# Kernel tuning notes

Hardware: AMD Instinct MI355X
Metric: run time of the kernel (lower is better)

Reference implementation:

```python
import jax, jax.numpy as jnp
import numpy as np

N_NODES = 50000
N_EDGES = 1600000
X_DIM = 128
HID = 128
HEADS = 8
C1 = HID // HEADS  # 16 per-head channels in gnn1
N_GRAPHS = 500
SLOPE = 0.3       # negative_slope (alpha in source)
BN_EPS = 1e-5


def segment_softmax(e, idx, n):
    # numerically stable softmax over segments defined by idx
    m = jax.ops.segment_max(e, idx, num_segments=n)
    ex = jnp.exp(e - m[idx])
    s = jax.ops.segment_sum(ex, idx, num_segments=n)
    return ex / (s[idx] + 1e-16)


def gatv2(x, src, dst, Wl, Wr, att, bias, heads, ch, concat):
    # PyG GATv2Conv (share_weights=False, edge_dim=None), eval mode (no dropout)
    n = x.shape[0]
    xl = (x @ Wl).reshape(n, heads, ch)  # messages (source side)
    xr = (x @ Wr).reshape(n, heads, ch)  # target side
    h = jax.nn.leaky_relu(xl[src] + xr[dst], SLOPE)      # [E,H,C]
    score = jnp.einsum('ehc,hc->eh', h, att)             # [E,H]
    alpha = segment_softmax(score, dst, n)               # softmax over in-edges of each target
    out = jax.ops.segment_sum(xl[src] * alpha[:, :, None], dst, num_segments=n)  # [N,H,C]
    out = out.reshape(n, heads * ch) if concat else out.mean(axis=1)
    return out + bias


def batchnorm_eval(x, g, b, rm, rv):
    return (x - rm) * (g / jnp.sqrt(rv + BN_EPS)) + b


def setup_inputs() -> dict:
    key = jax.random.key(0)
    ks = jax.random.split(key, 16)
    s = 0.05
    return {
        'x': jax.random.normal(ks[0], (N_NODES, X_DIM), jnp.float32),
        'edge_index': jax.random.randint(ks[1], (2, N_EDGES), 0, N_NODES, jnp.int32),
        'batch': jnp.sort(jax.random.randint(ks[2], (N_NODES,), 0, N_GRAPHS, jnp.int32)),
        # gnn1: GATv2Conv(x_dim -> hid//8, heads=8, concat)
        'Wl1': jax.random.normal(ks[3], (X_DIM, HID), jnp.float32) * s,
        'Wr1': jax.random.normal(ks[4], (X_DIM, HID), jnp.float32) * s,
        'att1': jax.random.normal(ks[5], (HEADS, C1), jnp.float32) * s,
        'b1': jnp.zeros((HID,), jnp.float32),
        # gnn2: GATv2Conv(hid -> hid, heads=1, concat=False)
        'Wl2': jax.random.normal(ks[6], (HID, HID), jnp.float32) * s,
        'Wr2': jax.random.normal(ks[7], (HID, HID), jnp.float32) * s,
        'att2': jax.random.normal(ks[8], (1, HID), jnp.float32) * s,
        'b2': jnp.zeros((HID,), jnp.float32),
        # shared BatchNorm1d(hid), eval mode buffers + affine
        'bn_g': jnp.ones((HID,), jnp.float32),
        'bn_b': jnp.zeros((HID,), jnp.float32),
        'bn_rm': jnp.zeros((HID,), jnp.float32),
        'bn_rv': jnp.ones((HID,), jnp.float32),
        # attentional aggregation gate_nn: Linear->Tanh->Linear(no bias)
        'Wg1': jax.random.normal(ks[9], (HID, HID), jnp.float32) * s,
        'bg1': jnp.zeros((HID,), jnp.float32),
        'Wg2': jax.random.normal(ks[10], (HID, 1), jnp.float32) * s,
        # fc_out: Linear(hid,100)->ReLU->Linear(100,1)
        'Wf1': jax.random.normal(ks[11], (HID, 100), jnp.float32) * s,
        'bf1': jnp.zeros((100,), jnp.float32),
        'Wf2': jax.random.normal(ks[12], (100, 1), jnp.float32) * s,
        'bf2': jnp.zeros((1,), jnp.float32),
    }


def reference(x, edge_index, batch, Wl1, Wr1, att1, b1, Wl2, Wr2, att2, b2,
              bn_g, bn_b, bn_rm, bn_rv, Wg1, bg1, Wg2, Wf1, bf1, Wf2, bf2):
    src, dst = edge_index[0], edge_index[1]
    # GAT layer 1 (8 heads, concat) -> dropout(eval no-op) -> BN -> ReLU
    h1 = gatv2(x, src, dst, Wl1, Wr1, att1, b1, HEADS, C1, True)
    h1 = jax.nn.relu(batchnorm_eval(h1, bn_g, bn_b, bn_rm, bn_rv))
    # GAT layer 2 (1 head, mean/no-concat) -> BN -> ReLU
    h2 = gatv2(h1, src, dst, Wl2, Wr2, att2, b2, 1, HID, False)
    h2 = jax.nn.relu(batchnorm_eval(h2, bn_g, bn_b, bn_rm, bn_rv))
    # AttentionalAggregation: softmax(gate_nn(x), batch) weighted sum
    gate = jnp.tanh(h2 @ Wg1 + bg1) @ Wg2                 # [N,1]
    gate = segment_softmax(gate, batch, N_GRAPHS)
    pooled = jax.ops.segment_sum(gate * h2, batch, num_segments=N_GRAPHS)  # [B,HID]
    # fc_out head
    return jax.nn.relu(pooled @ Wf1 + bf1) @ Wf2 + bf2    # [B,1]
```

## Files before the change

kernel.cpp:

```cpp
#include <hip/hip_runtime.h>
#include <math.h>

#define NEG_SLOPE 0.3f
#define BN_EPS 1e-5f
#define DEG_CAP 96

static __device__ __forceinline__ int lower_bound_i(const int* __restrict__ a, int n, int v) {
  int lo = 0, hi = n;
  while (lo < hi) {
    int mid = (lo + hi) >> 1;
    if (a[mid] < v) lo = mid + 1; else hi = mid;
  }
  return lo;
}

__global__ __launch_bounds__(256) void gemm2_kernel(const float* __restrict__ A,
    const float* __restrict__ W1, const float* __restrict__ W2,
    float* __restrict__ C1, float* __restrict__ C2, int n,
    const int* __restrict__ src, const int* __restrict__ dst, int ne,
    int* __restrict__ cursor, int* __restrict__ csr_src,
    const float* __restrict__ b1, const float* __restrict__ b2,
    const float* __restrict__ g, const float* __restrict__ bb,
    const float* __restrict__ rm, const float* __restrict__ rv,
    float* __restrict__ s1, float* __restrict__ h1s,
    float* __restrict__ s2, float* __restrict__ h2s,
    int gemm_blocks, int total_gs) {
  __shared__ float As[64 * 128];
  if (blockIdx.x >= total_gs) {
    int t = threadIdx.x;
    int c = t & 127;
    float s = g[c] / sqrtf(rv[c] + BN_EPS);
    const float* bias = (t < 128) ? b1 : b2;
    float* so = (t < 128) ? s1 : s2;
    float* ho = (t < 128) ? h1s : h2s;
    so[c] = s;
    ho[c] = (bias[c] - rm[c]) * s + bb[c];
    return;
  }
  if (blockIdx.x >= gemm_blocks) {
    int tid = (blockIdx.x - gemm_blocks) * 256 + threadIdx.x;
    int stride = (total_gs - gemm_blocks) * 256;
    int nb4 = ne >> 2;
    const int4* s4p = (const int4*)src;
    const int4* d4p = (const int4*)dst;
    for (int i = tid; i < nb4; i += stride) {
      int4 s4 = s4p[i];
      int4 d4 = d4p[i];
      csr_src[d4.x * DEG_CAP + atomicAdd(&cursor[d4.x], 1)] = s4.x;
      csr_src[d4.y * DEG_CAP + atomicAdd(&cursor[d4.y], 1)] = s4.y;
      csr_src[d4.z * DEG_CAP + atomicAdd(&cursor[d4.z], 1)] = s4.z;
      csr_src[d4.w * DEG_CAP + atomicAdd(&cursor[d4.w], 1)] = s4.w;
    }
    for (int i = (nb4 << 2) + tid; i < ne; i += stride) {
      int d = dst[i];
      csr_src[d * DEG_CAP + atomicAdd(&cursor[d], 1)] = src[i];
    }
    return;
  }
  int t = threadIdx.x;
  int r0 = blockIdx.x << 6;
  {
    float4* Asv = (float4*)As;
    if (r0 + 64 <= n) {
      const float4* Av = (const float4*)(A + (size_t)r0 * 128);
#pragma unroll
      for (int i = 0; i < 8; ++i) Asv[t + 256 * i] = Av[t + 256 * i];
    } else {
#pragma unroll
      for (int i = 0; i < 8; ++i) {
        int idx = t + 256 * i;
        int rr = idx >> 5;
        int cc = idx & 31;
        int gr = min(r0 + rr, n - 1);
        Asv[idx] = ((const float4*)(A + (size_t)gr * 128))[cc];
      }
    }
  }
  __syncthreads();
  int cg = t & 31;
  int rg = t >> 5;
  const float4* W1v = (const float4*)W1;
  const float4* W2v = (const float4*)W2;
  float4 a1[8], a2[8];
#pragma unroll
  for (int r = 0; r < 8; ++r) {
    a1[r] = make_float4(0.f, 0.f, 0.f, 0.f);
    a2[r] = make_float4(0.f, 0.f, 0.f, 0.f);
  }
  float4 u0 = W1v[0 * 32 + cg], u1 = W1v[1 * 32 + cg];
  float4 u2 = W1v[2 * 32 + cg], u3 = W1v[3 * 32 + cg];
  float4 v0 = W2v[0 * 32 + cg], v1 = W2v[1 * 32 + cg];
  float4 v2 = W2v[2 * 32 + cg], v3 = W2v[3 * 32 + cg];
#pragma unroll 2
  for (int kg = 0; kg < 32; ++kg) {
    int k = kg << 2;
    int kn = (kg < 31) ? (k + 4) : 0;
    float4 nu0 = W1v[(kn + 0) * 32 + cg];
    float4 nu1 = W1v[(kn + 1) * 32 + cg];
    float4 nu2 = W1v[(kn + 2) * 32 + cg];
    float4 nu3 = W1v[(kn + 3) * 32 + cg];
    float4 nv0 = W2v[(kn + 0) * 32 + cg];
    float4 nv1 = W2v[(kn + 1) * 32 + cg];
    float4 nv2 = W2v[(kn + 2) * 32 + cg];
    float4 nv3 = W2v[(kn + 3) * 32 + cg];
#pragma unroll
    for (int r = 0; r < 8; ++r) {
      float4 av = *(const float4*)&As[(rg * 8 + r) * 128 + k];
      a1[r].x += av.x * u0.x + av.y * u1.x + av.z * u2.x + av.w * u3.x;
      a1[r].y += av.x * u0.y + av.y * u1.y + av.z * u2.y + av.w * u3.y;
      a1[r].z += av.x * u0.z + av.y * u1.z + av.z * u2.z + av.w * u3.z;
      a1[r].w += av.x * u0.w + av.y * u1.w + av.z * u2.w + av.w * u3.w;
      a2[r].x += av.x * v0.x + av.y * v1.x + av.z * v2.x + av.w * v3.x;
      a2[r].y += av.x * v0.y + av.y * v1.y + av.z * v2.y + av.w * v3.y;
      a2[r].z += av.x * v0.z + av.y * v1.z + av.z * v2.z + av.w * v3.z;
      a2[r].w += av.x * v0.w + av.y * v1.w + av.z * v2.w + av.w * v3.w;
    }
    u0 = nu0; u1 = nu1; u2 = nu2; u3 = nu3;
    v0 = nv0; v1 = nv1; v2 = nv2; v3 = nv3;
  }
#pragma unroll
  for (int r = 0; r < 8; ++r) {
    int gr = r0 + rg * 8 + r;
    if (gr < n) {
      *(float4*)&C1[(size_t)gr * 128 + cg * 4] = a1[r];
      *(float4*)&C2[(size_t)gr * 128 + cg * 4] = a2[r];
    }
  }
}

__global__ __launch_bounds__(256) void gate_kernel(const float* __restrict__ A,
    const float* __restrict__ Wg1, const float* __restrict__ bg1,
    const float* __restrict__ Wg2, float* __restrict__ gate, int n) {
  __shared__ float As[64 * 128];
  int t = threadIdx.x;
  int r0 = blockIdx.x << 6;
  {
    float4* Asv = (float4*)As;
    if (r0 + 64 <= n) {
      const float4* Av = (const float4*)(A + (size_t)r0 * 128);
#pragma unroll
      for (int i = 0; i < 8; ++i) Asv[t + 256 * i] = Av[t + 256 * i];
    } else {
#pragma unroll
      for (int i = 0; i < 8; ++i) {
        int idx = t + 256 * i;
        int rr = idx >> 5;
        int cc = idx & 31;
        int gr = min(r0 + rr, n - 1);
        Asv[idx] = ((const float4*)(A + (size_t)gr * 128))[cc];
      }
    }
  }
  __syncthreads();
  int cg = t & 31;
  int rg = t >> 5;
  const float4* Wv = (const float4*)Wg1;
  float4 bg4 = *(const float4*)&bg1[cg * 4];
  float4 wg4 = *(const float4*)&Wg2[cg * 4];
  float4 acc[8];
#pragma unroll
  for (int r = 0; r < 8; ++r) acc[r] = make_float4(0.f, 0.f, 0.f, 0.f);
  float4 w0 = Wv[0 * 32 + cg];
  float4 w1 = Wv[1 * 32 + cg];
  float4 w2 = Wv[2 * 32 + cg];
  float4 w3 = Wv[3 * 32 + cg];
#pragma unroll 4
  for (int kg = 0; kg < 32; ++kg) {
    int k = kg << 2;
    int kn = (kg < 31) ? (k + 4) : 0;
    float4 nw0 = Wv[(kn + 0) * 32 + cg];
    float4 nw1 = Wv[(kn + 1) * 32 + cg];
    float4 nw2 = Wv[(kn + 2) * 32 + cg];
    float4 nw3 = Wv[(kn + 3) * 32 + cg];
#pragma unroll
    for (int r = 0; r < 8; ++r) {
      float4 av = *(const float4*)&As[(rg * 8 + r) * 128 + k];
      acc[r].x += av.x * w0.x + av.y * w1.x + av.z * w2.x + av.w * w3.x;
      acc[r].y += av.x * w0.y + av.y * w1.y + av.z * w2.y + av.w * w3.y;
      acc[r].z += av.x * w0.z + av.y * w1.z + av.z * w2.z + av.w * w3.z;
      acc[r].w += av.x * w0.w + av.y * w1.w + av.z * w2.w + av.w * w3.w;
    }
    w0 = nw0; w1 = nw1; w2 = nw2; w3 = nw3;
  }
#pragma unroll
  for (int r = 0; r < 8; ++r) {
    float v = tanhf(acc[r].x + bg4.x) * wg4.x
            + tanhf(acc[r].y + bg4.y) * wg4.y
            + tanhf(acc[r].z + bg4.z) * wg4.z
            + tanhf(acc[r].w + bg4.w) * wg4.w;
    v += __shfl_xor(v, 1);
    v += __shfl_xor(v, 2);
    v += __shfl_xor(v, 4);
    v += __shfl_xor(v, 8);
    v += __shfl_xor(v, 16);
    int gr = r0 + rg * 8 + r;
    if (cg == 0 && gr < n) gate[gr] = v;
  }
}

template<bool REDUCE>
__global__ __launch_bounds__(64) void gat_fused(
    const float* __restrict__ xl, const float* __restrict__ xr,
    const int* __restrict__ csr_src, const int* __restrict__ deg,
    const float* __restrict__ att,
    const float* __restrict__ bnscale, const float* __restrict__ bnshift,
    float* __restrict__ out, int n_nodes) {
  int n = blockIdx.x;
  if (n >= n_nodes) return;
  int l = threadIdx.x;
  int c = l & 7;
  int es = l >> 3;
  int co = c * 16;

  float4 at4[4], xr4[4];
  {
    const float4* atp = (const float4*)(att + co);
    const float4* xrp = (const float4*)(xr + (size_t)n * 128 + co);
#pragma unroll
    for (int j = 0; j < 4; ++j) { at4[j] = atp[j]; xr4[j] = xrp[j]; }
  }
  int d = deg[n];
  float acc[16];
#pragma unroll
  for (int j = 0; j < 16; ++j) acc[j] = 0.f;
  float ssum = 0.f;

  const int* cp = csr_src + (size_t)n * DEG_CAP;
  int iters = (d + 7) >> 3;

  auto loadgrp = [&](int eidx, float4* v) -> bool {
    bool valid = eidx < d;
    int ecl = valid ? eidx : (d - 1);
    int sidx = cp[ecl];
    const float4* xp = (const float4*)(xl + (size_t)sidx * 128 + co);
#pragma unroll
    for (int j = 0; j < 4; ++j) v[j] = xp[j];
    return valid;
  };
  auto compute = [&](const float4* v, bool valid) {
    float p = 0.f;
#pragma unroll
    for (int j = 0; j < 4; ++j) {
      float t0 = v[j].x + xr4[j].x;
      float t1 = v[j].y + xr4[j].y;
      float t2 = v[j].z + xr4[j].z;
      float t3 = v[j].w + xr4[j].w;
      p += at4[j].x * (fmaxf(t0, 0.f) + NEG_SLOPE * fminf(t0, 0.f));
      p += at4[j].y * (fmaxf(t1, 0.f) + NEG_SLOPE * fminf(t1, 0.f));
      p += at4[j].z * (fmaxf(t2, 0.f) + NEG_SLOPE * fminf(t2, 0.f));
      p += at4[j].w * (fmaxf(t3, 0.f) + NEG_SLOPE * fminf(t3, 0.f));
    }
    if (REDUCE) {
      p += __shfl_xor(p, 1);
      p += __shfl_xor(p, 2);
      p += __shfl_xor(p, 4);
    }
    float ex = valid ? __expf(p) : 0.f;
    ssum += ex;
#pragma unroll
    for (int j = 0; j < 4; ++j) {
      acc[4 * j + 0] += ex * v[j].x;
      acc[4 * j + 1] += ex * v[j].y;
      acc[4 * j + 2] += ex * v[j].z;
      acc[4 * j + 3] += ex * v[j].w;
    }
  };

  int i = 0;
  for (; i + 2 <= iters; i += 2) {
    float4 v0[4], v1[4];
    bool a = loadgrp((i << 3) + es, v0);
    bool b = loadgrp(((i + 1) << 3) + es, v1);
    compute(v0, a);
    compute(v1, b);
  }
  if (i < iters) {
    float4 v0[4];
    bool a = loadgrp((i << 3) + es, v0);
    compute(v0, a);
  }

#pragma unroll
  for (int st = 8; st <= 32; st <<= 1) {
    ssum += __shfl_xor(ssum, st);
#pragma unroll
    for (int j = 0; j < 16; ++j) acc[j] += __shfl_xor(acc[j], st);
  }

  if (es == 0) {
    float inv = 1.f / (ssum + 1e-16f);
    const float4* scp = (const float4*)(bnscale + co);
    const float4* shp = (const float4*)(bnshift + co);
    float4* op = (float4*)(out + (size_t)n * 128 + co);
#pragma unroll
    for (int j = 0; j < 4; ++j) {
      float4 sc = scp[j], sh = shp[j];
      float4 o;
      o.x = fmaxf(acc[4 * j + 0] * inv * sc.x + sh.x, 0.f);
      o.y = fmaxf(acc[4 * j + 1] * inv * sc.y + sh.y, 0.f);
      o.z = fmaxf(acc[4 * j + 2] * inv * sc.z + sh.z, 0.f);
      o.w = fmaxf(acc[4 * j + 3] * inv * sc.w + sh.w, 0.f);
      op[j] = o;
    }
  }
}

__global__ __launch_bounds__(128) void poolfc_kernel(const float* __restrict__ gate,
    const float* __restrict__ h2, const int* __restrict__ batch, int n_nodes,
    const float* __restrict__ Wf1, const float* __restrict__ bf1,
    const float* __restrict__ Wf2, const float* __restrict__ bf2,
    float* __restrict__ out, int n_graphs) {
  int g = blockIdx.x;
  if (g >= n_graphs) return;
  int t = threadIdx.x;
  int start = lower_bound_i(batch, n_nodes, g);
  int end = lower_bound_i(batch, n_nodes, g + 1);
  __shared__ float red[128];
  __shared__ float pl[128];
  float m = -__builtin_inff();
  for (int i = start + t; i < end; i += 128) m = fmaxf(m, gate[i]);
  red[t] = m;
  __syncthreads();
  for (int off = 64; off >= 1; off >>= 1) {
    if (t < off) red[t] = fmaxf(red[t], red[t + off]);
    __syncthreads();
  }
  m = red[0];
  __syncthreads();
  float s = 0.f, acc = 0.f;
  for (int i = start; i < end; ++i) {
    float ex = __expf(gate[i] - m);
    s += ex;
    acc += ex * h2[(size_t)i * 128 + t];
  }
  pl[t] = acc / (s + 1e-16f);
  __syncthreads();
  float v = 0.f;
  if (t < 100) {
    float a = bf1[t];
    for (int k = 0; k < 128; ++k) a += pl[k] * Wf1[k * 100 + t];
    v = fmaxf(a, 0.f) * Wf2[t];
  }
  red[t] = v;
  __syncthreads();
  for (int off = 64; off >= 1; off >>= 1) {
    if (t < off) red[t] += red[t + off];
    __syncthreads();
  }
  if (t == 0) out[g] = red[0] + bf2[0];
}

extern "C" void kernel_launch(void* const* d_in, const int* in_sizes, int n_in,
                              void* d_out, int out_size, void* d_ws, size_t ws_size,
                              hipStream_t stream) {
  const float* x     = (const float*)d_in[0];
  const int*   ei    = (const int*)d_in[1];
  const int*   batch = (const int*)d_in[2];
  const float* Wl1   = (const float*)d_in[3];
  const float* Wr1   = (const float*)d_in[4];
  const float* att1  = (const float*)d_in[5];
  const float* b1    = (const float*)d_in[6];
  const float* Wl2   = (const float*)d_in[7];
  const float* Wr2   = (const float*)d_in[8];
  const float* att2  = (const float*)d_in[9];
  const float* b2    = (const float*)d_in[10];
  const float* bn_g  = (const float*)d_in[11];
  const float* bn_b  = (const float*)d_in[12];
  const float* bn_rm = (const float*)d_in[13];
  const float* bn_rv = (const float*)d_in[14];
  const float* Wg1   = (const float*)d_in[15];
  const float* bg1   = (const float*)d_in[16];
  const float* Wg2   = (const float*)d_in[17];
  const float* Wf1   = (const float*)d_in[18];
  const float* bf1   = (const float*)d_in[19];
  const float* Wf2   = (const float*)d_in[20];
  const float* bf2   = (const float*)d_in[21];

  const int N  = in_sizes[0] / 128;
  const int E  = in_sizes[1] / 2;
  const int NG = out_size;
  const int* src = ei;
  const int* dst = ei + E;

  char* p = (char*)d_ws;
  auto alloc = [&](size_t bytes) -> void* {
    void* r = (void*)p;
    p += (bytes + 255) & ~(size_t)255;
    return r;
  };
  float* bufA    = (float*)alloc((size_t)N * 128 * 4);
  float* bufB    = (float*)alloc((size_t)N * 128 * 4);
  float* h1      = (float*)alloc((size_t)N * 128 * 4);
  int*   cursor  = (int*)alloc((size_t)N * 4);
  int*   csr_src = (int*)alloc((size_t)N * DEG_CAP * 4);
  float* gate    = (float*)alloc((size_t)N * 4);
  float* bns1    = (float*)alloc(128 * 4);
  float* bnh1    = (float*)alloc(128 * 4);
  float* bns2    = (float*)alloc(128 * 4);
  float* bnh2    = (float*)alloc(128 * 4);
  float* h2      = h1;

  const int gemm_blocks = (N + 63) >> 6;
  const int scat_blocks = 512;
  const int total_gs = gemm_blocks + scat_blocks;

  hipMemsetAsync(cursor, 0, (size_t)N * 4, stream);
  gemm2_kernel<<<total_gs + 1, 256, 0, stream>>>(
      x, Wl1, Wr1, bufA, bufB, N, src, dst, E, cursor, csr_src,
      b1, b2, bn_g, bn_b, bn_rm, bn_rv, bns1, bnh1, bns2, bnh2,
      gemm_blocks, total_gs);
  gat_fused<false><<<N, 64, 0, stream>>>(bufA, bufB, csr_src, cursor, att1,
                                         bns1, bnh1, h1, N);
  gemm2_kernel<<<gemm_blocks, 256, 0, stream>>>(
      h1, Wl2, Wr2, bufA, bufB, N, nullptr, nullptr, 0, nullptr, nullptr,
      nullptr, nullptr, nullptr, nullptr, nullptr, nullptr,
      nullptr, nullptr, nullptr, nullptr, gemm_blocks, gemm_blocks);
  gat_fused<true><<<N, 64, 0, stream>>>(bufA, bufB, csr_src, cursor, att2,
                                        bns2, bnh2, h2, N);
  gate_kernel<<<gemm_blocks, 256, 0, stream>>>(h2, Wg1, bg1, Wg2, gate, N);
  poolfc_kernel<<<NG, 128, 0, stream>>>(gate, h2, batch, N, Wf1, bf1, Wf2, bf2,
                                        (float*)d_out, NG);
}
```

Measured before the change: 577.5 us.

## Fuse gate MLP into per-graph pooling kernel and double scatter blocks

Removes the separate gate GEMM kernel and computes the tanh gate MLP inside the per-graph pooling kernel, four nodes at a time, keeping gate values in shared memory. This saves one launch and the global gate buffer round trip. The cost is that only 500 blocks of 128 threads do the gate GEMM with poor reuse: one scalar per k, Wg1 read from global, and a sync per 4 rows. Gate storage is capped at 512 nodes per graph, which silently truncates larger graphs. The scatter block count in the first GEMM kernel is also doubled.

```diff
diff --git a/kernel.cpp b/kernel.cpp
--- a/kernel.cpp
+++ b/kernel.cpp
@@ -128,76 +128,6 @@
   }
 }
 
-__global__ __launch_bounds__(256) void gate_kernel(const float* __restrict__ A,
-    const float* __restrict__ Wg1, const float* __restrict__ bg1,
-    const float* __restrict__ Wg2, float* __restrict__ gate, int n) {
-  __shared__ float As[64 * 128];
-  int t = threadIdx.x;
-  int r0 = blockIdx.x << 6;
-  {
-    float4* Asv = (float4*)As;
-    if (r0 + 64 <= n) {
-      const float4* Av = (const float4*)(A + (size_t)r0 * 128);
-#pragma unroll
-      for (int i = 0; i < 8; ++i) Asv[t + 256 * i] = Av[t + 256 * i];
-    } else {
-#pragma unroll
-      for (int i = 0; i < 8; ++i) {
-        int idx = t + 256 * i;
-        int rr = idx >> 5;
-        int cc = idx & 31;
-        int gr = min(r0 + rr, n - 1);
-        Asv[idx] = ((const float4*)(A + (size_t)gr * 128))[cc];
-      }
-    }
-  }
-  __syncthreads();
-  int cg = t & 31;
-  int rg = t >> 5;
-  const float4* Wv = (const float4*)Wg1;
-  float4 bg4 = *(const float4*)&bg1[cg * 4];
-  float4 wg4 = *(const float4*)&Wg2[cg * 4];
-  float4 acc[8];
-#pragma unroll
-  for (int r = 0; r < 8; ++r) acc[r] = make_float4(0.f, 0.f, 0.f, 0.f);
-  float4 w0 = Wv[0 * 32 + cg];
-  float4 w1 = Wv[1 * 32 + cg];
-  float4 w2 = Wv[2 * 32 + cg];
-  float4 w3 = Wv[3 * 32 + cg];
-#pragma unroll 4
-  for (int kg = 0; kg < 32; ++kg) {
-    int k = kg << 2;
-    int kn = (kg < 31) ? (k + 4) : 0;
-    float4 nw0 = Wv[(kn + 0) * 32 + cg];
-    float4 nw1 = Wv[(kn + 1) * 32 + cg];
-    float4 nw2 = Wv[(kn + 2) * 32 + cg];
-    float4 nw3 = Wv[(kn + 3) * 32 + cg];
-#pragma unroll
-    for (int r = 0; r < 8; ++r) {
-      float4 av = *(const float4*)&As[(rg * 8 + r) * 128 + k];
-      acc[r].x += av.x * w0.x + av.y * w1.x + av.z * w2.x + av.w * w3.x;
-      acc[r].y += av.x * w0.y + av.y * w1.y + av.z * w2.y + av.w * w3.y;
-      acc[r].z += av.x * w0.z + av.y * w1.z + av.z * w2.z + av.w * w3.z;
-      acc[r].w += av.x * w0.w + av.y * w1.w + av.z * w2.w + av.w * w3.w;
-    }
-    w0 = nw0; w1 = nw1; w2 = nw2; w3 = nw3;
-  }
-#pragma unroll
-  for (int r = 0; r < 8; ++r) {
-    float v = tanhf(acc[r].x + bg4.x) * wg4.x
-            + tanhf(acc[r].y + bg4.y) * wg4.y
-            + tanhf(acc[r].z + bg4.z) * wg4.z
-            + tanhf(acc[r].w + bg4.w) * wg4.w;
-    v += __shfl_xor(v, 1);
-    v += __shfl_xor(v, 2);
-    v += __shfl_xor(v, 4);
-    v += __shfl_xor(v, 8);
-    v += __shfl_xor(v, 16);
-    int gr = r0 + rg * 8 + r;
-    if (cg == 0 && gr < n) gate[gr] = v;
-  }
-}
-
 template<bool REDUCE>
 __global__ __launch_bounds__(64) void gat_fused(
     const float* __restrict__ xl, const float* __restrict__ xr,
@@ -305,8 +235,10 @@
   }
 }
 
-__global__ __launch_bounds__(128) void poolfc_kernel(const float* __restrict__ gate,
+__global__ __launch_bounds__(128) void gatepool_kernel(
     const float* __restrict__ h2, const int* __restrict__ batch, int n_nodes,
+    const float* __restrict__ Wg1, const float* __restrict__ bg1,
+    const float* __restrict__ Wg2,
     const float* __restrict__ Wf1, const float* __restrict__ bf1,
     const float* __restrict__ Wf2, const float* __restrict__ bf2,
     float* __restrict__ out, int n_graphs) {
@@ -315,10 +247,53 @@
   int t = threadIdx.x;
   int start = lower_bound_i(batch, n_nodes, g);
   int end = lower_bound_i(batch, n_nodes, g + 1);
+  int cnt = end - start;
+  __shared__ float As[8 * 128];
+  __shared__ float gatev[512];
   __shared__ float red[128];
   __shared__ float pl[128];
+
+  int cg = t & 31;
+  int rg = t >> 5;
+  float4 bg4 = *(const float4*)&bg1[cg * 4];
+  float4 wg4 = *(const float4*)&Wg2[cg * 4];
+  for (int i0 = 0; i0 < cnt; i0 += 4) {
+    {
+      float4* Asv = (float4*)As;
+      int idx = t;
+      if (idx < 128) {
+        int rr = idx >> 5;
+        int cc = idx & 31;
+        int gr = start + min(i0 + rr, cnt - 1);
+        Asv[idx] = ((const float4*)(h2 + (size_t)gr * 128))[cc];
+      }
+    }
+    __syncthreads();
+    float4 acc = make_float4(0.f, 0.f, 0.f, 0.f);
+#pragma unroll 4
+    for (int k = 0; k < 128; ++k) {
+      float av = As[rg * 128 + k];
+      float4 w = *(const float4*)&Wg1[k * 128 + cg * 4];
+      acc.x += av * w.x;
+      acc.y += av * w.y;
+      acc.z += av * w.z;
+      acc.w += av * w.w;
+    }
+    float v = tanhf(acc.x + bg4.x) * wg4.x
+            + tanhf(acc.y + bg4.y) * wg4.y
+            + tanhf(acc.z + bg4.z) * wg4.z
+            + tanhf(acc.w + bg4.w) * wg4.w;
+    v += __shfl_xor(v, 1);
+    v += __shfl_xor(v, 2);
+    v += __shfl_xor(v, 4);
+    v += __shfl_xor(v, 8);
+    v += __shfl_xor(v, 16);
+    __syncthreads();
+    if (cg == 0 && (i0 + rg) < cnt && (i0 + rg) < 512) gatev[i0 + rg] = v;
+  }
+  __syncthreads();
   float m = -__builtin_inff();
-  for (int i = start + t; i < end; i += 128) m = fmaxf(m, gate[i]);
+  for (int i = t; i < cnt; i += 128) m = fmaxf(m, gatev[i]);
   red[t] = m;
   __syncthreads();
   for (int off = 64; off >= 1; off >>= 1) {
@@ -328,10 +303,10 @@
   m = red[0];
   __syncthreads();
   float s = 0.f, acc = 0.f;
-  for (int i = start; i < end; ++i) {
-    float ex = __expf(gate[i] - m);
+  for (int i = 0; i < cnt; ++i) {
+    float ex = __expf(gatev[i] - m);
     s += ex;
-    acc += ex * h2[(size_t)i * 128 + t];
+    acc += ex * h2[(size_t)(start + i) * 128 + t];
   }
   pl[t] = acc / (s + 1e-16f);
   __syncthreads();
@@ -393,7 +368,6 @@
   float* h1      = (float*)alloc((size_t)N * 128 * 4);
   int*   cursor  = (int*)alloc((size_t)N * 4);
   int*   csr_src = (int*)alloc((size_t)N * DEG_CAP * 4);
-  float* gate    = (float*)alloc((size_t)N * 4);
   float* bns1    = (float*)alloc(128 * 4);
   float* bnh1    = (float*)alloc(128 * 4);
   float* bns2    = (float*)alloc(128 * 4);
@@ -401,7 +375,7 @@
   float* h2      = h1;
 
   const int gemm_blocks = (N + 63) >> 6;
-  const int scat_blocks = 512;
+  const int scat_blocks = 1024;
   const int total_gs = gemm_blocks + scat_blocks;
 
   hipMemsetAsync(cursor, 0, (size_t)N * 4, stream);
@@ -417,7 +391,6 @@
       nullptr, nullptr, nullptr, nullptr, gemm_blocks, gemm_blocks);
   gat_fused<true><<<N, 64, 0, stream>>>(bufA, bufB, csr_src, cursor, att2,
                                         bns2, bnh2, h2, N);
-  gate_kernel<<<gemm_blocks, 256, 0, stream>>>(h2, Wg1, bg1, Wg2, gate, N);
-  poolfc_kernel<<<NG, 128, 0, stream>>>(gate, h2, batch, N, Wf1, bf1, Wf2, bf2,
-                                        (float*)d_out, NG);
-}
+  gatepool_kernel<<<NG, 128, 0, stream>>>(h2, batch, N, Wg1, bg1, Wg2,
+                                          Wf1, bf1, Wf2, bf2, (float*)d_out, NG);
+}
```

Result: slower. 677.2 us (+17.3%).
